# Performance work log

Measured on AMD Instinct MI355X. Metric: run time of the kernel, lower is better.

## Reference

```python
import jax, jax.numpy as jnp
import numpy as np

N_NODES = 100000
N_EDGES = 1600000
F_IN = 128
F_HID = 16


def _gcn_conv(x, src, dst, W, b, n):
    # PyG GCNConv: x' = D^{-1/2} (A + I) D^{-1/2} (x W) + b
    h = x @ W                                   # [N, F_out] transform first (small F)
    deg = jax.ops.segment_sum(jnp.ones_like(dst, dtype=h.dtype), dst, num_segments=n)
    dinv = jnp.where(deg > 0, jax.lax.rsqrt(deg), 0.0)
    norm = dinv[src] * dinv[dst]                # [E+N] edge weights
    msg = h[src] * norm[:, None]                # gather + scale
    out = jax.ops.segment_sum(msg, dst, num_segments=n)  # scatter-add
    return out + b


def setup_inputs() -> dict:
    key = jax.random.key(0)
    k1, k2, k3, k4 = jax.random.split(key, 4)
    x = jax.random.normal(k1, (N_NODES, F_IN), dtype=jnp.float32)
    edge_index = jax.random.randint(k2, (2, N_EDGES), 0, N_NODES, dtype=jnp.int64)
    # Glorot-ish init for the two GCNConv weights
    W1 = jax.random.normal(k3, (F_IN, F_HID), dtype=jnp.float32) * (1.0 / np.sqrt(F_IN))
    b1 = jnp.zeros((F_HID,), dtype=jnp.float32)
    W2 = jax.random.normal(k4, (F_HID, F_IN), dtype=jnp.float32) * (1.0 / np.sqrt(F_HID))
    b2 = jnp.zeros((F_IN,), dtype=jnp.float32)
    return {"x": x, "edge_index": edge_index, "W1": W1, "b1": b1, "W2": W2, "b2": b2}


def reference(x, edge_index, W1, b1, W2, b2):
    n = x.shape[0]
    # add self-loops once (GCNConv default add_self_loops=True)
    loop = jnp.arange(n, dtype=edge_index.dtype)
    src = jnp.concatenate([edge_index[0], loop])
    dst = jnp.concatenate([edge_index[1], loop])
    h = _gcn_conv(x, src, dst, W1, b1, n)
    h = jax.nn.relu(h)
    out = _gcn_conv(h, src, dst, W2, b2, n)
    return out
```

## Files before the change

kernel.cpp:

```cpp
#include <hip/hip_runtime.h>
#include <hip/hip_fp16.h>


#define NN 100000
#define NE 1600000
#define FI 128
#define FH 16
#define CB 64
#define NB 1563
#define GC 512
#define CHUNK 3125
#define SCB 16

__device__ __forceinline__ float fc(const float4& v, int i) {
    return i == 0 ? v.x : i == 1 ? v.y : i == 2 ? v.z : v.w;
}

__global__ __launch_bounds__(256) void k_count_gemm1(const int* __restrict__ dst,
                                                     int* __restrict__ hist,
                                                     const float* __restrict__ x,
                                                     const float* __restrict__ W1,
                                                     __half2* __restrict__ g1) {
    __shared__ int h[NB];
    __shared__ __align__(16) float w[FI * FH];
    if (blockIdx.x < GC) {
        for (int i = threadIdx.x; i < NB; i += 256) h[i] = 0;
        __syncthreads();
        int base = blockIdx.x * CHUNK;
        for (int i = base + threadIdx.x; i < base + CHUNK; i += 256)
            atomicAdd(&h[dst[i] >> 6], 1);
        __syncthreads();
        for (int b = threadIdx.x; b < NB; b += 256)
            hist[blockIdx.x * NB + b] = h[b];
    } else {
        float4* w4s = (float4*)w;
        w4s[threadIdx.x] = ((const float4*)W1)[threadIdx.x];
        w4s[threadIdx.x + 256] = ((const float4*)W1)[threadIdx.x + 256];
        __syncthreads();
        int fg = threadIdx.x & 3;
        int ng = threadIdx.x >> 2;
        int r0 = (blockIdx.x - GC) * 256 + ng * 4;
        const float4* x4 = (const float4*)x;
        int rr[4]; bool val[4];
        #pragma unroll
        for (int i = 0; i < 4; ++i) {
            val[i] = (r0 + i < NN);
            rr[i] = val[i] ? r0 + i : NN - 1;
        }
        float acc[4][4];
        #pragma unroll
        for (int i = 0; i < 4; ++i)
            #pragma unroll
            for (int j = 0; j < 4; ++j) acc[i][j] = 0.f;
        #pragma unroll 2
        for (int k4 = 0; k4 < 32; ++k4) {
            float4 xv[4];
            #pragma unroll
            for (int i = 0; i < 4; ++i) xv[i] = x4[rr[i] * 32 + k4];
            #pragma unroll
            for (int kk = 0; kk < 4; ++kk) {
                float4 wv = w4s[(k4 * 4 + kk) * 4 + fg];
                #pragma unroll
                for (int i = 0; i < 4; ++i) {
                    float xk = fc(xv[i], kk);
                    acc[i][0] += xk * wv.x; acc[i][1] += xk * wv.y;
                    acc[i][2] += xk * wv.z; acc[i][3] += xk * wv.w;
                }
            }
        }
        #pragma unroll
        for (int i = 0; i < 4; ++i) if (val[i]) {
            g1[rr[i] * 8 + fg * 2]     = __floats2half2_rn(acc[i][0], acc[i][1]);
            g1[rr[i] * 8 + fg * 2 + 1] = __floats2half2_rn(acc[i][2], acc[i][3]);
        }
    }
}

__global__ __launch_bounds__(256) void k_scan_chunks(int* __restrict__ hist,
                                                     int* __restrict__ totals) {
    __shared__ int s[GC * SCB];
    int b0 = blockIdx.x * SCB;
    int o[GC * SCB / 256];
    #pragma unroll
    for (int r = 0; r < GC * SCB / 256; ++r) {
        int idx = r * 256 + threadIdx.x;
        int c = idx >> 4, bl = idx & (SCB - 1), b = b0 + bl;
        int v = (b < NB) ? hist[c * NB + b] : 0;
        s[idx] = v;
        o[r] = v;
    }
    __syncthreads();
    for (int off = 1; off < GC; off <<= 1) {
        int t[GC * SCB / 256];
        #pragma unroll
        for (int r = 0; r < GC * SCB / 256; ++r) {
            int idx = r * 256 + threadIdx.x;
            int c = idx >> 4;
            t[r] = (c >= off) ? s[idx - off * SCB] : 0;
        }
        __syncthreads();
        #pragma unroll
        for (int r = 0; r < GC * SCB / 256; ++r) {
            int idx = r * 256 + threadIdx.x;
            s[idx] += t[r];
        }
        __syncthreads();
    }
    #pragma unroll
    for (int r = 0; r < GC * SCB / 256; ++r) {
        int idx = r * 256 + threadIdx.x;
        int c = idx >> 4, bl = idx & (SCB - 1), b = b0 + bl;
        if (b < NB) {
            hist[c * NB + b] = s[idx] - o[r];
            if (c == GC - 1) totals[b] = s[idx];
        }
    }
}

__global__ __launch_bounds__(1024) void k_scan_buckets(const int* __restrict__ totals,
                                                       int* __restrict__ bucketStart,
                                                       int* __restrict__ rowStart) {
    __shared__ int s[1024];
    int tid = threadIdx.x;
    int i0 = 2 * tid, i1 = i0 + 1;
    int a = (i0 < NB) ? totals[i0] : 0;
    int b = (i1 < NB) ? totals[i1] : 0;
    s[tid] = a + b;
    __syncthreads();
    #pragma unroll
    for (int off = 1; off < 1024; off <<= 1) {
        int t = (tid >= off) ? s[tid - off] : 0;
        __syncthreads();
        s[tid] += t;
        __syncthreads();
    }
    int excl = s[tid] - (a + b);
    if (i0 < NB) bucketStart[i0] = excl;
    if (i1 < NB) bucketStart[i1] = excl + a;
    if (tid == 0) { bucketStart[NB] = NE; rowStart[NN] = NE; }
}

__global__ __launch_bounds__(256) void k_scatter(const int* __restrict__ src,
                                                 const int* __restrict__ dst,
                                                 const int* __restrict__ hist,
                                                 const int* __restrict__ bucketStart,
                                                 int* __restrict__ packed) {
    __shared__ int cur[NB];
    for (int b = threadIdx.x; b < NB; b += 256)
        cur[b] = hist[blockIdx.x * NB + b] + bucketStart[b];
    __syncthreads();
    int base = blockIdx.x * CHUNK;
    for (int i = base + threadIdx.x; i < base + CHUNK; i += 256) {
        int d = dst[i];
        int pos = atomicAdd(&cur[d >> 6], 1);
        packed[pos] = src[i] | ((d & 63) << 17);
    }
}

__global__ __launch_bounds__(256) void k_bsort(const int* __restrict__ packed,
                                               const int* __restrict__ bucketStart,
                                               int* __restrict__ csr,
                                               int* __restrict__ rowStart,
                                               float* __restrict__ dinv) {
    __shared__ int cnt[CB];
    __shared__ int rs[CB];
    __shared__ int cur[CB];
    if (threadIdx.x < CB) cnt[threadIdx.x] = 0;
    __syncthreads();
    int s0 = bucketStart[blockIdx.x], s1 = bucketStart[blockIdx.x + 1];
    for (int i = s0 + threadIdx.x; i < s1; i += 256)
        atomicAdd(&cnt[(packed[i] >> 17) & 63], 1);
    __syncthreads();
    if (threadIdx.x < CB) rs[threadIdx.x] = cnt[threadIdx.x];
    __syncthreads();
    #pragma unroll
    for (int off = 1; off < CB; off <<= 1) {
        int t = 0;
        if (threadIdx.x < CB && threadIdx.x >= off) t = rs[threadIdx.x - off];
        __syncthreads();
        if (threadIdx.x < CB) rs[threadIdx.x] += t;
        __syncthreads();
    }
    if (threadIdx.x < CB) {
        int start = s0 + rs[threadIdx.x] - cnt[threadIdx.x];
        cur[threadIdx.x] = start;
        int node = blockIdx.x * CB + threadIdx.x;
        if (node < NN) {
            rowStart[node] = start;
            dinv[node] = rsqrtf((float)(cnt[threadIdx.x] + 1));
        }
    }
    __syncthreads();
    for (int i = s0 + threadIdx.x; i < s1; i += 256) {
        int pk = packed[i];
        int pos = atomicAdd(&cur[(pk >> 17) & 63], 1);
        csr[pos] = pk & 131071;
    }
}

__global__ __launch_bounds__(256) void k_agg1(const int* __restrict__ csr,
                                              const int* __restrict__ rowStart,
                                              const __half2* __restrict__ g1,
                                              const float* __restrict__ dinv,
                                              const float* __restrict__ b1,
                                              __half2* __restrict__ g2) {
    int gid = blockIdx.x * 256 + threadIdx.x;
    int node = gid >> 3, c = gid & 7;
    if (node >= NN) return;
    int s0 = rowStart[node], s1 = rowStart[node + 1];
    float dv = dinv[node];
    float2 fs = __half22float2(g1[node * 8 + c]);
    float2 acc = make_float2(dv * fs.x, dv * fs.y);
    int e = s0;
    for (; e + 3 < s1; e += 4) {
        int i0 = csr[e], i1 = csr[e + 1], i2 = csr[e + 2], i3 = csr[e + 3];
        float d0 = dinv[i0], d1 = dinv[i1], d2 = dinv[i2], d3 = dinv[i3];
        float2 f0 = __half22float2(g1[i0 * 8 + c]);
        float2 f1 = __half22float2(g1[i1 * 8 + c]);
        float2 f2 = __half22float2(g1[i2 * 8 + c]);
        float2 f3 = __half22float2(g1[i3 * 8 + c]);
        acc.x = fmaf(d0, f0.x, fmaf(d1, f1.x, fmaf(d2, f2.x, fmaf(d3, f3.x, acc.x))));
        acc.y = fmaf(d0, f0.y, fmaf(d1, f1.y, fmaf(d2, f2.y, fmaf(d3, f3.y, acc.y))));
    }
    for (; e < s1; ++e) {
        int i0 = csr[e];
        float d0 = dinv[i0];
        float2 f = __half22float2(g1[i0 * 8 + c]);
        acc.x = fmaf(d0, f.x, acc.x);
        acc.y = fmaf(d0, f.y, acc.y);
    }
    float2 bb = *(const float2*)(b1 + 2 * c);
    float vx = fmaxf(dv * acc.x + bb.x, 0.f) * dv;
    float vy = fmaxf(dv * acc.y + bb.y, 0.f) * dv;
    g2[node * 8 + c] = __floats2half2_rn(vx, vy);
}

__global__ __launch_bounds__(256) void k_aggemm2(const int* __restrict__ csr,
                                                 const int* __restrict__ rowStart,
                                                 const float* __restrict__ dinv,
                                                 const __half2* __restrict__ g2,
                                                 const float* __restrict__ W2,
                                                 const float* __restrict__ b2,
                                                 float* __restrict__ out) {
    __shared__ __align__(16) float w[FH * FI];
    __shared__ __align__(16) float pst[FH][32];
    float4* w4s = (float4*)w;
    w4s[threadIdx.x] = ((const float4*)W2)[threadIdx.x];
    w4s[threadIdx.x + 256] = ((const float4*)W2)[threadIdx.x + 256];
    int base = blockIdx.x * 32;
    int ln = threadIdx.x >> 3, c = threadIdx.x & 7;
    int node = base + ln;
    float2 acc = make_float2(0.f, 0.f);
    if (node < NN) {
        int s0 = rowStart[node], s1 = rowStart[node + 1];
        acc = __half22float2(g2[node * 8 + c]);
        int e = s0;
        for (; e + 3 < s1; e += 4) {
            int i0 = csr[e], i1 = csr[e + 1], i2 = csr[e + 2], i3 = csr[e + 3];
            float2 f0 = __half22float2(g2[i0 * 8 + c]);
            float2 f1 = __half22float2(g2[i1 * 8 + c]);
            float2 f2 = __half22float2(g2[i2 * 8 + c]);
            float2 f3 = __half22float2(g2[i3 * 8 + c]);
            acc.x += (f0.x + f1.x) + (f2.x + f3.x);
            acc.y += (f0.y + f1.y) + (f2.y + f3.y);
        }
        for (; e < s1; ++e) {
            float2 f = __half22float2(g2[csr[e] * 8 + c]);
            acc.x += f.x; acc.y += f.y;
        }
        float dv = dinv[node];
        acc.x *= dv; acc.y *= dv;
    }
    pst[2 * c][ln]     = acc.x;
    pst[2 * c + 1][ln] = acc.y;
    __syncthreads();
    int fg = threadIdx.x & 31;
    int ng = threadIdx.x >> 5;
    float4 bb = ((const float4*)b2)[fg];
    float a2[4][4];
    #pragma unroll
    for (int i = 0; i < 4; ++i) {
        a2[i][0] = bb.x; a2[i][1] = bb.y; a2[i][2] = bb.z; a2[i][3] = bb.w;
    }
    #pragma unroll
    for (int k = 0; k < FH; ++k) {
        float4 xk = *(float4*)&pst[k][ng * 4];
        float4 wv = w4s[k * 32 + fg];
        #pragma unroll
        for (int i = 0; i < 4; ++i) {
            float xv = fc(xk, i);
            a2[i][0] += xv * wv.x; a2[i][1] += xv * wv.y;
            a2[i][2] += xv * wv.z; a2[i][3] += xv * wv.w;
        }
    }
    #pragma unroll
    for (int i = 0; i < 4; ++i) {
        int gn = base + ng * 4 + i;
        if (gn < NN)
            ((float4*)out)[gn * 32 + fg] =
                make_float4(a2[i][0], a2[i][1], a2[i][2], a2[i][3]);
    }
}

extern "C" void kernel_launch(void* const* d_in, const int* in_sizes, int n_in,
                              void* d_out, int out_size, void* d_ws, size_t ws_size,
                              hipStream_t stream) {
    const float* x  = (const float*)d_in[0];
    const int*   ei = (const int*)d_in[1];
    const float* W1 = (const float*)d_in[2];
    const float* b1 = (const float*)d_in[3];
    const float* W2 = (const float*)d_in[4];
    const float* b2 = (const float*)d_in[5];
    float* out = (float*)d_out;

    const int* src = ei;
    const int* dst = ei + NE;

    int*   totals      = (int*)d_ws;
    int*   bucketStart = totals + NB;
    int*   rowStart    = bucketStart + NB + 1;
    float* dinv        = (float*)(rowStart + NN + 1);
    int*   csr         = (int*)(dinv + NN);
    int*   hist        = csr;
    int*   packed      = csr + NE;
    __half2* g1        = (__half2*)(packed + NE);
    __half2* g2        = g1 + NN * 8;

    k_count_gemm1 <<<GC + (NN + 255) / 256, 256, 0, stream>>>(dst, hist, x, W1, g1);
    k_scan_chunks <<<(NB + SCB - 1) / SCB, 256, 0, stream>>>(hist, totals);
    k_scan_buckets<<<1, 1024, 0, stream>>>(totals, bucketStart, rowStart);
    k_scatter     <<<GC, 256, 0, stream>>>(src, dst, hist, bucketStart, packed);
    k_bsort       <<<NB, 256, 0, stream>>>(packed, bucketStart, csr, rowStart, dinv);
    k_agg1        <<<(NN * 8) / 256, 256, 0, stream>>>(csr, rowStart, g1, dinv, b1, g2);
    k_aggemm2     <<<(NN + 31) / 32, 256, 0, stream>>>(csr, rowStart, dinv, g2, W2, b2, out);
}
```

Baseline: 247.1 us.

## Prescale g1 by dinv in bsort and widen aggregation gathers to 8-byte loads

```diff
diff --git a/kernel.cpp b/kernel.cpp
--- a/kernel.cpp
+++ b/kernel.cpp
@@ -16,14 +16,16 @@
     return i == 0 ? v.x : i == 1 ? v.y : i == 2 ? v.z : v.w;
 }
 
+struct h2x2 { __half2 a, b; };
+
 __global__ __launch_bounds__(256) void k_count_gemm1(const int* __restrict__ dst,
                                                      int* __restrict__ hist,
                                                      const float* __restrict__ x,
                                                      const float* __restrict__ W1,
                                                      __half2* __restrict__ g1) {
-    __shared__ int h[NB];
     __shared__ __align__(16) float w[FI * FH];
     if (blockIdx.x < GC) {
+        int* h = (int*)w;
         for (int i = threadIdx.x; i < NB; i += 256) h[i] = 0;
         __syncthreads();
         int base = blockIdx.x * CHUNK;
@@ -161,10 +163,12 @@
                                                const int* __restrict__ bucketStart,
                                                int* __restrict__ csr,
                                                int* __restrict__ rowStart,
-                                               float* __restrict__ dinv) {
+                                               float* __restrict__ dinv,
+                                               __half2* __restrict__ g1) {
     __shared__ int cnt[CB];
     __shared__ int rs[CB];
     __shared__ int cur[CB];
+    __shared__ float dvs[CB];
     if (threadIdx.x < CB) cnt[threadIdx.x] = 0;
     __syncthreads();
     int s0 = bucketStart[blockIdx.x], s1 = bucketStart[blockIdx.x + 1];
@@ -184,10 +188,12 @@
     if (threadIdx.x < CB) {
         int start = s0 + rs[threadIdx.x] - cnt[threadIdx.x];
         cur[threadIdx.x] = start;
+        float dv = rsqrtf((float)(cnt[threadIdx.x] + 1));
+        dvs[threadIdx.x] = dv;
         int node = blockIdx.x * CB + threadIdx.x;
         if (node < NN) {
             rowStart[node] = start;
-            dinv[node] = rsqrtf((float)(cnt[threadIdx.x] + 1));
+            dinv[node] = dv;
         }
     }
     __syncthreads();
@@ -195,6 +201,17 @@
         int pk = packed[i];
         int pos = atomicAdd(&cur[(pk >> 17) & 63], 1);
         csr[pos] = pk & 131071;
+    }
+    int gbase = blockIdx.x * (CB * 8);
+    #pragma unroll
+    for (int r = 0; r < 2; ++r) {
+        int i = r * 256 + threadIdx.x;
+        int gi = gbase + i;
+        if (gi < NN * 8) {
+            float dv = dvs[i >> 3];
+            float2 f = __half22float2(g1[gi]);
+            g1[gi] = __floats2half2_rn(f.x * dv, f.y * dv);
+        }
     }
 }
 
@@ -205,34 +222,41 @@
                                               const float* __restrict__ b1,
                                               __half2* __restrict__ g2) {
     int gid = blockIdx.x * 256 + threadIdx.x;
-    int node = gid >> 3, c = gid & 7;
+    int node = gid >> 2, c4 = gid & 3;
     if (node >= NN) return;
     int s0 = rowStart[node], s1 = rowStart[node + 1];
-    float dv = dinv[node];
-    float2 fs = __half22float2(g1[node * 8 + c]);
-    float2 acc = make_float2(dv * fs.x, dv * fs.y);
+    h2x2 sv = *(const h2x2*)(g1 + node * 8 + 2 * c4);
+    float2 a0 = __half22float2(sv.a);
+    float2 a1 = __half22float2(sv.b);
     int e = s0;
     for (; e + 3 < s1; e += 4) {
         int i0 = csr[e], i1 = csr[e + 1], i2 = csr[e + 2], i3 = csr[e + 3];
-        float d0 = dinv[i0], d1 = dinv[i1], d2 = dinv[i2], d3 = dinv[i3];
-        float2 f0 = __half22float2(g1[i0 * 8 + c]);
-        float2 f1 = __half22float2(g1[i1 * 8 + c]);
-        float2 f2 = __half22float2(g1[i2 * 8 + c]);
-        float2 f3 = __half22float2(g1[i3 * 8 + c]);
-        acc.x = fmaf(d0, f0.x, fmaf(d1, f1.x, fmaf(d2, f2.x, fmaf(d3, f3.x, acc.x))));
-        acc.y = fmaf(d0, f0.y, fmaf(d1, f1.y, fmaf(d2, f2.y, fmaf(d3, f3.y, acc.y))));
+        h2x2 v0 = *(const h2x2*)(g1 + i0 * 8 + 2 * c4);
+        h2x2 v1 = *(const h2x2*)(g1 + i1 * 8 + 2 * c4);
+        h2x2 v2 = *(const h2x2*)(g1 + i2 * 8 + 2 * c4);
+        h2x2 v3 = *(const h2x2*)(g1 + i3 * 8 + 2 * c4);
+        float2 f0 = __half22float2(v0.a), f1 = __half22float2(v1.a);
+        float2 f2 = __half22float2(v2.a), f3 = __half22float2(v3.a);
+        float2 h0 = __half22float2(v0.b), h1 = __half22float2(v1.b);
+        float2 h2 = __half22float2(v2.b), h3 = __half22float2(v3.b);
+        a0.x += (f0.x + f1.x) + (f2.x + f3.x);
+        a0.y += (f0.y + f1.y) + (f2.y + f3.y);
+        a1.x += (h0.x + h1.x) + (h2.x + h3.x);
+        a1.y += (h0.y + h1.y) + (h2.y + h3.y);
     }
     for (; e < s1; ++e) {
-        int i0 = csr[e];
-        float d0 = dinv[i0];
-        float2 f = __half22float2(g1[i0 * 8 + c]);
-        acc.x = fmaf(d0, f.x, acc.x);
-        acc.y = fmaf(d0, f.y, acc.y);
-    }
-    float2 bb = *(const float2*)(b1 + 2 * c);
-    float vx = fmaxf(dv * acc.x + bb.x, 0.f) * dv;
-    float vy = fmaxf(dv * acc.y + bb.y, 0.f) * dv;
-    g2[node * 8 + c] = __floats2half2_rn(vx, vy);
+        h2x2 v = *(const h2x2*)(g1 + csr[e] * 8 + 2 * c4);
+        float2 f = __half22float2(v.a), h = __half22float2(v.b);
+        a0.x += f.x; a0.y += f.y; a1.x += h.x; a1.y += h.y;
+    }
+    float dv = dinv[node];
+    float4 bb = *(const float4*)(b1 + 4 * c4);
+    h2x2 o;
+    o.a = __floats2half2_rn(fmaxf(dv * a0.x + bb.x, 0.f) * dv,
+                            fmaxf(dv * a0.y + bb.y, 0.f) * dv);
+    o.b = __floats2half2_rn(fmaxf(dv * a1.x + bb.z, 0.f) * dv,
+                            fmaxf(dv * a1.y + bb.w, 0.f) * dv);
+    *(h2x2*)(g2 + node * 8 + 2 * c4) = o;
 }
 
 __global__ __launch_bounds__(256) void k_aggemm2(const int* __restrict__ csr,
@@ -243,59 +267,69 @@
                                                  const float* __restrict__ b2,
                                                  float* __restrict__ out) {
     __shared__ __align__(16) float w[FH * FI];
-    __shared__ __align__(16) float pst[FH][32];
+    __shared__ float pst[FH][68];
     float4* w4s = (float4*)w;
     w4s[threadIdx.x] = ((const float4*)W2)[threadIdx.x];
     w4s[threadIdx.x + 256] = ((const float4*)W2)[threadIdx.x + 256];
-    int base = blockIdx.x * 32;
-    int ln = threadIdx.x >> 3, c = threadIdx.x & 7;
+    int base = blockIdx.x * 64;
+    int ln = threadIdx.x >> 2, c4 = threadIdx.x & 3;
     int node = base + ln;
-    float2 acc = make_float2(0.f, 0.f);
+    float2 a0 = make_float2(0.f, 0.f), a1 = make_float2(0.f, 0.f);
     if (node < NN) {
         int s0 = rowStart[node], s1 = rowStart[node + 1];
-        acc = __half22float2(g2[node * 8 + c]);
+        h2x2 sv = *(const h2x2*)(g2 + node * 8 + 2 * c4);
+        a0 = __half22float2(sv.a);
+        a1 = __half22float2(sv.b);
         int e = s0;
         for (; e + 3 < s1; e += 4) {
             int i0 = csr[e], i1 = csr[e + 1], i2 = csr[e + 2], i3 = csr[e + 3];
-            float2 f0 = __half22float2(g2[i0 * 8 + c]);
-            float2 f1 = __half22float2(g2[i1 * 8 + c]);
-            float2 f2 = __half22float2(g2[i2 * 8 + c]);
-            float2 f3 = __half22float2(g2[i3 * 8 + c]);
-            acc.x += (f0.x + f1.x) + (f2.x + f3.x);
-            acc.y += (f0.y + f1.y) + (f2.y + f3.y);
+            h2x2 v0 = *(const h2x2*)(g2 + i0 * 8 + 2 * c4);
+            h2x2 v1 = *(const h2x2*)(g2 + i1 * 8 + 2 * c4);
+            h2x2 v2 = *(const h2x2*)(g2 + i2 * 8 + 2 * c4);
+            h2x2 v3 = *(const h2x2*)(g2 + i3 * 8 + 2 * c4);
+            float2 f0 = __half22float2(v0.a), f1 = __half22float2(v1.a);
+            float2 f2 = __half22float2(v2.a), f3 = __half22float2(v3.a);
+            float2 h0 = __half22float2(v0.b), h1 = __half22float2(v1.b);
+            float2 h2 = __half22float2(v2.b), h3 = __half22float2(v3.b);
+            a0.x += (f0.x + f1.x) + (f2.x + f3.x);
+            a0.y += (f0.y + f1.y) + (f2.y + f3.y);
+            a1.x += (h0.x + h1.x) + (h2.x + h3.x);
+            a1.y += (h0.y + h1.y) + (h2.y + h3.y);
         }
         for (; e < s1; ++e) {
-            float2 f = __half22float2(g2[csr[e] * 8 + c]);
-            acc.x += f.x; acc.y += f.y;
+            h2x2 v = *(const h2x2*)(g2 + csr[e] * 8 + 2 * c4);
+            float2 f = __half22float2(v.a), h = __half22float2(v.b);
+            a0.x += f.x; a0.y += f.y; a1.x += h.x; a1.y += h.y;
         }
         float dv = dinv[node];
-        acc.x *= dv; acc.y *= dv;
-    }
-    pst[2 * c][ln]     = acc.x;
-    pst[2 * c + 1][ln] = acc.y;
+        a0.x *= dv; a0.y *= dv; a1.x *= dv; a1.y *= dv;
+    }
+    pst[4 * c4 + 0][ln] = a0.x;
+    pst[4 * c4 + 1][ln] = a0.y;
+    pst[4 * c4 + 2][ln] = a1.x;
+    pst[4 * c4 + 3][ln] = a1.y;
     __syncthreads();
     int fg = threadIdx.x & 31;
     int ng = threadIdx.x >> 5;
     float4 bb = ((const float4*)b2)[fg];
-    float a2[4][4];
-    #pragma unroll
-    for (int i = 0; i < 4; ++i) {
+    float a2[8][4];
+    #pragma unroll
+    for (int i = 0; i < 8; ++i) {
         a2[i][0] = bb.x; a2[i][1] = bb.y; a2[i][2] = bb.z; a2[i][3] = bb.w;
     }
     #pragma unroll
     for (int k = 0; k < FH; ++k) {
-        float4 xk = *(float4*)&pst[k][ng * 4];
         float4 wv = w4s[k * 32 + fg];
         #pragma unroll
-        for (int i = 0; i < 4; ++i) {
-            float xv = fc(xk, i);
+        for (int i = 0; i < 8; ++i) {
+            float xv = pst[k][ng * 8 + i];
             a2[i][0] += xv * wv.x; a2[i][1] += xv * wv.y;
             a2[i][2] += xv * wv.z; a2[i][3] += xv * wv.w;
         }
     }
     #pragma unroll
-    for (int i = 0; i < 4; ++i) {
-        int gn = base + ng * 4 + i;
+    for (int i = 0; i < 8; ++i) {
+        int gn = base + ng * 8 + i;
         if (gn < NN)
             ((float4*)out)[gn * 32 + fg] =
                 make_float4(a2[i][0], a2[i][1], a2[i][2], a2[i][3]);
@@ -330,7 +364,7 @@
     k_scan_chunks <<<(NB + SCB - 1) / SCB, 256, 0, stream>>>(hist, totals);
     k_scan_buckets<<<1, 1024, 0, stream>>>(totals, bucketStart, rowStart);
     k_scatter     <<<GC, 256, 0, stream>>>(src, dst, hist, bucketStart, packed);
-    k_bsort       <<<NB, 256, 0, stream>>>(packed, bucketStart, csr, rowStart, dinv);
-    k_agg1        <<<(NN * 8) / 256, 256, 0, stream>>>(csr, rowStart, g1, dinv, b1, g2);
-    k_aggemm2     <<<(NN + 31) / 32, 256, 0, stream>>>(csr, rowStart, dinv, g2, W2, b2, out);
-}
+    k_bsort       <<<NB, 256, 0, stream>>>(packed, bucketStart, csr, rowStart, dinv, g1);
+    k_agg1        <<<(NN * 4 + 255) / 256, 256, 0, stream>>>(csr, rowStart, g1, dinv, b1, g2);
+    k_aggemm2     <<<(NN + 63) / 64, 256, 0, stream>>>(csr, rowStart, dinv, g2, W2, b2, out);
+}
```

After: 245.3 us. No clear change (-0.7%).

## Pad CSR rows to multiples of four with dummy node and split aggregation from GEMM2

Applied to the files above, without the earlier changes.

```diff
diff --git a/kernel.cpp b/kernel.cpp
--- a/kernel.cpp
+++ b/kernel.cpp
@@ -21,9 +21,9 @@
                                                      const float* __restrict__ x,
                                                      const float* __restrict__ W1,
                                                      __half2* __restrict__ g1) {
-    __shared__ int h[NB];
     __shared__ __align__(16) float w[FI * FH];
     if (blockIdx.x < GC) {
+        int* h = (int*)w;
         for (int i = threadIdx.x; i < NB; i += 256) h[i] = 0;
         __syncthreads();
         int base = blockIdx.x * CHUNK;
@@ -119,9 +119,10 @@
 
 __global__ __launch_bounds__(1024) void k_scan_buckets(const int* __restrict__ totals,
                                                        int* __restrict__ bucketStart,
-                                                       int* __restrict__ rowStart) {
+                                                       __half2* __restrict__ g1) {
     __shared__ int s[1024];
     int tid = threadIdx.x;
+    if (tid < 8) g1[NN * 8 + tid] = __floats2half2_rn(0.f, 0.f);
     int i0 = 2 * tid, i1 = i0 + 1;
     int a = (i0 < NB) ? totals[i0] : 0;
     int b = (i1 < NB) ? totals[i1] : 0;
@@ -137,7 +138,7 @@
     int excl = s[tid] - (a + b);
     if (i0 < NB) bucketStart[i0] = excl;
     if (i1 < NB) bucketStart[i1] = excl + a;
-    if (tid == 0) { bucketStart[NB] = NE; rowStart[NN] = NE; }
+    if (tid == 0) bucketStart[NB] = NE;
 }
 
 __global__ __launch_bounds__(256) void k_scatter(const int* __restrict__ src,
@@ -160,34 +161,45 @@
 __global__ __launch_bounds__(256) void k_bsort(const int* __restrict__ packed,
                                                const int* __restrict__ bucketStart,
                                                int* __restrict__ csr,
-                                               int* __restrict__ rowStart,
-                                               float* __restrict__ dinv) {
+                                               int2* __restrict__ rowSE,
+                                               float* __restrict__ dinv,
+                                               __half2* __restrict__ g1) {
     __shared__ int cnt[CB];
-    __shared__ int rs[CB];
+    __shared__ int rsp[CB];
     __shared__ int cur[CB];
+    __shared__ float dvs[CB];
+    int b = blockIdx.x;
     if (threadIdx.x < CB) cnt[threadIdx.x] = 0;
     __syncthreads();
-    int s0 = bucketStart[blockIdx.x], s1 = bucketStart[blockIdx.x + 1];
+    int s0 = bucketStart[b], s1 = bucketStart[b + 1];
     for (int i = s0 + threadIdx.x; i < s1; i += 256)
         atomicAdd(&cnt[(packed[i] >> 17) & 63], 1);
     __syncthreads();
-    if (threadIdx.x < CB) rs[threadIdx.x] = cnt[threadIdx.x];
+    int c = 0, cp = 0;
+    if (threadIdx.x < CB) {
+        c = cnt[threadIdx.x];
+        cp = (c + 3) & ~3;
+        rsp[threadIdx.x] = cp;
+    }
     __syncthreads();
     #pragma unroll
     for (int off = 1; off < CB; off <<= 1) {
         int t = 0;
-        if (threadIdx.x < CB && threadIdx.x >= off) t = rs[threadIdx.x - off];
-        __syncthreads();
-        if (threadIdx.x < CB) rs[threadIdx.x] += t;
-        __syncthreads();
-    }
+        if (threadIdx.x < CB && threadIdx.x >= off) t = rsp[threadIdx.x - off];
+        __syncthreads();
+        if (threadIdx.x < CB) rsp[threadIdx.x] += t;
+        __syncthreads();
+    }
+    int base = (s0 + 200 * b + 3) & ~3;
     if (threadIdx.x < CB) {
-        int start = s0 + rs[threadIdx.x] - cnt[threadIdx.x];
+        int start = base + rsp[threadIdx.x] - cp;
         cur[threadIdx.x] = start;
-        int node = blockIdx.x * CB + threadIdx.x;
+        float dv = rsqrtf((float)(c + 1));
+        dvs[threadIdx.x] = dv;
+        int node = b * CB + threadIdx.x;
         if (node < NN) {
-            rowStart[node] = start;
-            dinv[node] = rsqrtf((float)(cnt[threadIdx.x] + 1));
+            rowSE[node] = make_int2(start, start + cp);
+            dinv[node] = dv;
         }
     }
     __syncthreads();
@@ -196,83 +208,94 @@
         int pos = atomicAdd(&cur[(pk >> 17) & 63], 1);
         csr[pos] = pk & 131071;
     }
+    __syncthreads();
+    if (threadIdx.x < CB) {
+        int end = cur[threadIdx.x];
+        int endp = end + (cp - c);
+        for (int p = end; p < endp; ++p) csr[p] = NN;
+    }
+    int gbase = b * (CB * 8);
+    #pragma unroll
+    for (int r = 0; r < 2; ++r) {
+        int i = r * 256 + threadIdx.x;
+        int gi = gbase + i;
+        if (gi < NN * 8) {
+            float dv = dvs[i >> 3];
+            float2 f = __half22float2(g1[gi]);
+            g1[gi] = __floats2half2_rn(f.x * dv, f.y * dv);
+        }
+    }
 }
 
 __global__ __launch_bounds__(256) void k_agg1(const int* __restrict__ csr,
-                                              const int* __restrict__ rowStart,
+                                              const int2* __restrict__ rowSE,
                                               const __half2* __restrict__ g1,
                                               const float* __restrict__ dinv,
                                               const float* __restrict__ b1,
                                               __half2* __restrict__ g2) {
+    if (blockIdx.x == 0 && threadIdx.x < 8)
+        g2[NN * 8 + threadIdx.x] = __floats2half2_rn(0.f, 0.f);
     int gid = blockIdx.x * 256 + threadIdx.x;
     int node = gid >> 3, c = gid & 7;
     if (node >= NN) return;
-    int s0 = rowStart[node], s1 = rowStart[node + 1];
+    int2 se = rowSE[node];
+    float2 acc = __half22float2(g1[node * 8 + c]);
+    for (int e = se.x; e < se.y; e += 4) {
+        int4 i4 = *(const int4*)(csr + e);
+        float2 f0 = __half22float2(g1[i4.x * 8 + c]);
+        float2 f1 = __half22float2(g1[i4.y * 8 + c]);
+        float2 f2 = __half22float2(g1[i4.z * 8 + c]);
+        float2 f3 = __half22float2(g1[i4.w * 8 + c]);
+        acc.x += (f0.x + f1.x) + (f2.x + f3.x);
+        acc.y += (f0.y + f1.y) + (f2.y + f3.y);
+    }
     float dv = dinv[node];
-    float2 fs = __half22float2(g1[node * 8 + c]);
-    float2 acc = make_float2(dv * fs.x, dv * fs.y);
-    int e = s0;
-    for (; e + 3 < s1; e += 4) {
-        int i0 = csr[e], i1 = csr[e + 1], i2 = csr[e + 2], i3 = csr[e + 3];
-        float d0 = dinv[i0], d1 = dinv[i1], d2 = dinv[i2], d3 = dinv[i3];
-        float2 f0 = __half22float2(g1[i0 * 8 + c]);
-        float2 f1 = __half22float2(g1[i1 * 8 + c]);
-        float2 f2 = __half22float2(g1[i2 * 8 + c]);
-        float2 f3 = __half22float2(g1[i3 * 8 + c]);
-        acc.x = fmaf(d0, f0.x, fmaf(d1, f1.x, fmaf(d2, f2.x, fmaf(d3, f3.x, acc.x))));
-        acc.y = fmaf(d0, f0.y, fmaf(d1, f1.y, fmaf(d2, f2.y, fmaf(d3, f3.y, acc.y))));
-    }
-    for (; e < s1; ++e) {
-        int i0 = csr[e];
-        float d0 = dinv[i0];
-        float2 f = __half22float2(g1[i0 * 8 + c]);
-        acc.x = fmaf(d0, f.x, acc.x);
-        acc.y = fmaf(d0, f.y, acc.y);
-    }
     float2 bb = *(const float2*)(b1 + 2 * c);
-    float vx = fmaxf(dv * acc.x + bb.x, 0.f) * dv;
-    float vy = fmaxf(dv * acc.y + bb.y, 0.f) * dv;
-    g2[node * 8 + c] = __floats2half2_rn(vx, vy);
-}
-
-__global__ __launch_bounds__(256) void k_aggemm2(const int* __restrict__ csr,
-                                                 const int* __restrict__ rowStart,
-                                                 const float* __restrict__ dinv,
-                                                 const __half2* __restrict__ g2,
-                                                 const float* __restrict__ W2,
-                                                 const float* __restrict__ b2,
-                                                 float* __restrict__ out) {
+    g2[node * 8 + c] = __floats2half2_rn(fmaxf(dv * acc.x + bb.x, 0.f) * dv,
+                                         fmaxf(dv * acc.y + bb.y, 0.f) * dv);
+}
+
+__global__ __launch_bounds__(256) void k_agg2(const int* __restrict__ csr,
+                                              const int2* __restrict__ rowSE,
+                                              const __half2* __restrict__ g2,
+                                              const float* __restrict__ dinv,
+                                              __half2* __restrict__ p2h) {
+    int gid = blockIdx.x * 256 + threadIdx.x;
+    int node = gid >> 3, c = gid & 7;
+    if (node >= NN) return;
+    int2 se = rowSE[node];
+    float2 acc = __half22float2(g2[node * 8 + c]);
+    for (int e = se.x; e < se.y; e += 4) {
+        int4 i4 = *(const int4*)(csr + e);
+        float2 f0 = __half22float2(g2[i4.x * 8 + c]);
+        float2 f1 = __half22float2(g2[i4.y * 8 + c]);
+        float2 f2 = __half22float2(g2[i4.z * 8 + c]);
+        float2 f3 = __half22float2(g2[i4.w * 8 + c]);
+        acc.x += (f0.x + f1.x) + (f2.x + f3.x);
+        acc.y += (f0.y + f1.y) + (f2.y + f3.y);
+    }
+    float dv = dinv[node];
+    p2h[node * 8 + c] = __floats2half2_rn(dv * acc.x, dv * acc.y);
+}
+
+__global__ __launch_bounds__(256) void k_gemm2(const __half2* __restrict__ p2h,
+                                               const float* __restrict__ W2,
+                                               const float* __restrict__ b2,
+                                               float* __restrict__ out) {
     __shared__ __align__(16) float w[FH * FI];
-    __shared__ __align__(16) float pst[FH][32];
+    __shared__ float pst[FH][33];
     float4* w4s = (float4*)w;
     w4s[threadIdx.x] = ((const float4*)W2)[threadIdx.x];
     w4s[threadIdx.x + 256] = ((const float4*)W2)[threadIdx.x + 256];
     int base = blockIdx.x * 32;
-    int ln = threadIdx.x >> 3, c = threadIdx.x & 7;
-    int node = base + ln;
-    float2 acc = make_float2(0.f, 0.f);
-    if (node < NN) {
-        int s0 = rowStart[node], s1 = rowStart[node + 1];
-        acc = __half22float2(g2[node * 8 + c]);
-        int e = s0;
-        for (; e + 3 < s1; e += 4) {
-            int i0 = csr[e], i1 = csr[e + 1], i2 = csr[e + 2], i3 = csr[e + 3];
-            float2 f0 = __half22float2(g2[i0 * 8 + c]);
-            float2 f1 = __half22float2(g2[i1 * 8 + c]);
-            float2 f2 = __half22float2(g2[i2 * 8 + c]);
-            float2 f3 = __half22float2(g2[i3 * 8 + c]);
-            acc.x += (f0.x + f1.x) + (f2.x + f3.x);
-            acc.y += (f0.y + f1.y) + (f2.y + f3.y);
-        }
-        for (; e < s1; ++e) {
-            float2 f = __half22float2(g2[csr[e] * 8 + c]);
-            acc.x += f.x; acc.y += f.y;
-        }
-        float dv = dinv[node];
-        acc.x *= dv; acc.y *= dv;
-    }
-    pst[2 * c][ln]     = acc.x;
-    pst[2 * c + 1][ln] = acc.y;
+    {
+        int n = threadIdx.x >> 3, cc = threadIdx.x & 7;
+        int gn = base + n;
+        __half2 hv = (gn < NN) ? p2h[gn * 8 + cc] : __floats2half2_rn(0.f, 0.f);
+        float2 f = __half22float2(hv);
+        pst[2 * cc][n]     = f.x;
+        pst[2 * cc + 1][n] = f.y;
+    }
     __syncthreads();
     int fg = threadIdx.x & 31;
     int ng = threadIdx.x >> 5;
@@ -284,11 +307,10 @@
     }
     #pragma unroll
     for (int k = 0; k < FH; ++k) {
-        float4 xk = *(float4*)&pst[k][ng * 4];
         float4 wv = w4s[k * 32 + fg];
         #pragma unroll
         for (int i = 0; i < 4; ++i) {
-            float xv = fc(xk, i);
+            float xv = pst[k][ng * 4 + i];
             a2[i][0] += xv * wv.x; a2[i][1] += xv * wv.y;
             a2[i][2] += xv * wv.z; a2[i][3] += xv * wv.w;
         }
@@ -316,21 +338,23 @@
     const int* src = ei;
     const int* dst = ei + NE;
 
-    int*   totals      = (int*)d_ws;
+    int2*  rowSE       = (int2*)d_ws;
+    float* dinv        = (float*)(rowSE + NN);
+    int*   totals      = (int*)(dinv + NN);
     int*   bucketStart = totals + NB;
-    int*   rowStart    = bucketStart + NB + 1;
-    float* dinv        = (float*)(rowStart + NN + 1);
-    int*   csr         = (int*)(dinv + NN);
-    int*   hist        = csr;
-    int*   packed      = csr + NE;
-    __half2* g1        = (__half2*)(packed + NE);
-    __half2* g2        = g1 + NN * 8;
+    int*   csrPad      = bucketStart + NB + 1 + 1;
+    int*   hist        = csrPad;
+    int*   packed      = csrPad + (NE + 200 * NB);
+    __half2* g2        = (__half2*)packed;
+    __half2* p2h       = g2 + (NN + 1) * 8;
+    __half2* g1        = (__half2*)(packed + NE + 16);
 
     k_count_gemm1 <<<GC + (NN + 255) / 256, 256, 0, stream>>>(dst, hist, x, W1, g1);
     k_scan_chunks <<<(NB + SCB - 1) / SCB, 256, 0, stream>>>(hist, totals);
-    k_scan_buckets<<<1, 1024, 0, stream>>>(totals, bucketStart, rowStart);
+    k_scan_buckets<<<1, 1024, 0, stream>>>(totals, bucketStart, g1);
     k_scatter     <<<GC, 256, 0, stream>>>(src, dst, hist, bucketStart, packed);
-    k_bsort       <<<NB, 256, 0, stream>>>(packed, bucketStart, csr, rowStart, dinv);
-    k_agg1        <<<(NN * 8) / 256, 256, 0, stream>>>(csr, rowStart, g1, dinv, b1, g2);
-    k_aggemm2     <<<(NN + 31) / 32, 256, 0, stream>>>(csr, rowStart, dinv, g2, W2, b2, out);
-}
+    k_bsort       <<<NB, 256, 0, stream>>>(packed, bucketStart, csrPad, rowSE, dinv, g1);
+    k_agg1        <<<(NN * 8) / 256, 256, 0, stream>>>(csrPad, rowSE, g1, dinv, b1, g2);
+    k_agg2        <<<(NN * 8) / 256, 256, 0, stream>>>(csrPad, rowSE, g2, dinv, p2h);
+    k_gemm2       <<<(NN + 31) / 32, 256, 0, stream>>>(p2h, W2, b2, out);
+}
```

Measured after the change: 233.3 us. -5.6%, faster.
